# Kernel tuning notes

Measured on AMD Instinct MI355X. Metric: run time of the kernel, lower is better.

## Reference

```python
import jax, jax.numpy as jnp
import numpy as np

B, S, D_IN, D_H = 8, 2048, 512, 512

def setup_inputs() -> dict:
    key = jax.random.key(0)
    ks = jax.random.split(key, 7)
    s = 1.0 / np.sqrt(D_IN)
    return {
        "x": jax.random.normal(ks[0], (B, S, D_IN), dtype=jnp.float32),
        "Wq": jax.random.uniform(ks[1], (D_H, D_IN), jnp.float32, -s, s),
        "bq": jax.random.uniform(ks[2], (D_H,), jnp.float32, -s, s),
        "Wk": jax.random.uniform(ks[3], (D_H, D_IN), jnp.float32, -s, s),
        "bk": jax.random.uniform(ks[4], (D_H,), jnp.float32, -s, s),
        "Wv": jax.random.uniform(ks[5], (D_H, D_IN), jnp.float32, -s, s),
        "bv": jax.random.uniform(ks[6], (D_H,), jnp.float32, -s, s),
    }

def reference(x, Wq, bq, Wk, bk, Wv, bv):
    # torch Linear: y = x @ W.T + b
    Q = jnp.einsum('bsd,hd->bsh', x, Wq) + bq
    K = jnp.einsum('bsd,hd->bsh', x, Wk) + bk
    V = jnp.einsum('bsd,hd->bsh', x, Wv) + bv
    scale = jnp.sqrt(jnp.asarray(D_H, dtype=x.dtype))
    scores = jnp.einsum('bqh,bkh->bqk', Q, K) / scale  # [B,S,S]
    attn = jax.nn.softmax(scores, axis=-1)
    return jnp.einsum('bqk,bkh->bqh', attn, V)
```

## Files before the change

kernel.cpp:

```cpp
#include <hip/hip_runtime.h>
#include <hip/hip_bf16.h>
#include <cstdint>

#define B_   8
#define S_   2048
#define DIN  512
#define DH   512

typedef __attribute__((ext_vector_type(8))) short  short8;
typedef __attribute__((ext_vector_type(4))) short  short4_;
typedef __attribute__((ext_vector_type(4))) float  float4_;

__device__ inline unsigned short f2bf(float f) {
    union { float f; unsigned u; } v; v.f = f;
    unsigned u = v.u;
    u += 0x7fffu + ((u >> 16) & 1u);
    return (unsigned short)(u >> 16);
}

__device__ inline void gload_lds16(const void* g, void* l) {
    __builtin_amdgcn_global_load_lds(
        (const __attribute__((address_space(1))) void*)g,
        (__attribute__((address_space(3))) void*)l, 16, 0, 0);
}

template <int C>
__device__ inline float fdpp(float x) {
    return __int_as_float(__builtin_amdgcn_update_dpp(0, __float_as_int(x), C, 0xF, 0xF, true));
}
__device__ inline float rsum16(float v) {
    v += fdpp<0x140>(v);
    v += fdpp<0x141>(v);
    v += fdpp<27>(v);
    v += fdpp<177>(v);
    return v;
}

__global__ __launch_bounds__(256) void conv_bf16(
    const float* __restrict__ x,
    const float* __restrict__ Wq, const float* __restrict__ Wk, const float* __restrict__ Wv,
    unsigned short* __restrict__ xb, unsigned short* __restrict__ wb)
{
    const int NX4 = (B_ * S_ * DIN) / 4;
    const int NW4 = (DH * DIN) / 4;
    const int total = NX4 + 3 * NW4;
    for (int i = blockIdx.x * blockDim.x + threadIdx.x; i < total;
         i += gridDim.x * blockDim.x) {
        const float4_* src; unsigned short* dst; int j;
        if (i < NX4)             { src = (const float4_*)x;  dst = xb;            j = i; }
        else if (i < NX4 + NW4)  { src = (const float4_*)Wq; dst = wb;            j = i - NX4; }
        else if (i < NX4 + 2*NW4){ src = (const float4_*)Wk; dst = wb + DH*DIN;   j = i - NX4 - NW4; }
        else                     { src = (const float4_*)Wv; dst = wb + 2*DH*DIN; j = i - NX4 - 2*NW4; }
        float4_ v = src[j];
        short4_ o;
        o[0] = (short)f2bf(v[0]); o[1] = (short)f2bf(v[1]);
        o[2] = (short)f2bf(v[2]); o[3] = (short)f2bf(v[3]);
        ((short4_*)dst)[j] = o;
    }
}

__global__ __launch_bounds__(256) void qkv_gemm(
    const unsigned short* __restrict__ xb,
    const unsigned short* __restrict__ wb,
    const float* __restrict__ bq, const float* __restrict__ bk, const float* __restrict__ bv,
    unsigned short* __restrict__ qws, unsigned short* __restrict__ kws,
    unsigned short* __restrict__ vt2)
{
    __shared__ __align__(16) unsigned short smem[17408];

    const int flat = blockIdx.y * 128 + blockIdx.x;
    const int swz  = (flat & 7) * 192 + (flat >> 3);
    const int tm   = swz / 12;
    const int tc   = swz % 12;
    const int mat  = tc >> 2;
    const int nb   = (tc & 3) * 128;
    const int tid  = threadIdx.x;
    const int w    = tid >> 6;
    const int lane = tid & 63;
    const int l15  = lane & 15;
    const int quad = lane >> 4;
    const int wm   = (w & 1) * 64;
    const int wn   = (w >> 1) * 64;
    const int m0   = tm * 128;

    const unsigned short* wmat = wb + (size_t)mat * DH * DIN;

    float4_ zero = {0.f, 0.f, 0.f, 0.f};
    float4_ acc[4][4];
    #pragma unroll
    for (int i = 0; i < 4; i++)
        #pragma unroll
        for (int j = 0; j < 4; j++) acc[i][j] = zero;

    const int lr = lane >> 2;
    const int lb = (lane & 3) * 16;

    auto stage = [&](int kk, int bufi) {
        unsigned short* Ab = smem + bufi * 8192;
        unsigned short* Bb = smem + 4096 + bufi * 8192;
        #pragma unroll
        for (int c = 0; c < 2; c++) {
            int r = w * 32 + c * 16;
            const unsigned char* gA = (const unsigned char*)(xb + (size_t)(m0 + r) * DIN + kk);
            gload_lds16(gA + (size_t)lr * (DIN * 2) + lb, (void*)(Ab + r * 32));
            const unsigned char* gB = (const unsigned char*)(wmat + (size_t)(nb + r) * DIN + kk);
            gload_lds16(gB + (size_t)lr * (DIN * 2) + lb, (void*)(Bb + r * 32));
        }
    };

    stage(0, 0);
    for (int ki = 0; ki < 16; ki++) {
        __syncthreads();
        if (ki < 15) stage((ki + 1) * 32, (ki + 1) & 1);
        const unsigned short* Ab = smem + (ki & 1) * 8192;
        const unsigned short* Bb = smem + 4096 + (ki & 1) * 8192;
        short8 af[4], bf[4];
        #pragma unroll
        for (int mt = 0; mt < 4; mt++)
            af[mt] = *(const short8*)(Ab + (wm + mt * 16 + l15) * 32 + quad * 8);
        #pragma unroll
        for (int nt = 0; nt < 4; nt++)
            bf[nt] = *(const short8*)(Bb + (wn + nt * 16 + l15) * 32 + quad * 8);
        #pragma unroll
        for (int mt = 0; mt < 4; mt++)
            #pragma unroll
            for (int nt = 0; nt < 4; nt++)
                acc[mt][nt] = __builtin_amdgcn_mfma_f32_16x16x32_bf16(af[mt], bf[nt], acc[mt][nt], 0, 0, 0);
    }

    if (mat < 2) {
        const float* bias  = (mat == 0) ? bq : bk;
        const float  scale = (mat == 0) ? 0.06375870430742225f : 1.0f;
        unsigned short* dst = (mat == 0) ? qws : kws;
        #pragma unroll
        for (int nt = 0; nt < 4; nt++) {
            int n = nb + wn + nt * 16 + l15;
            float bv_ = bias[n];
            #pragma unroll
            for (int mt = 0; mt < 4; mt++) {
                #pragma unroll
                for (int r = 0; r < 4; r++) {
                    int m = m0 + wm + mt * 16 + quad * 4 + r;
                    dst[(size_t)m * DH + n] = f2bf((acc[mt][nt][r] + bv_) * scale);
                }
            }
        }
    } else {
        __syncthreads();
        unsigned short* trans = smem;
        #pragma unroll
        for (int nt = 0; nt < 4; nt++) {
            int dloc = wn + nt * 16 + l15;
            float bv_ = bv[nb + dloc];
            #pragma unroll
            for (int mt = 0; mt < 4; mt++) {
                short4_ pk;
                #pragma unroll
                for (int r = 0; r < 4; r++) pk[r] = (short)f2bf(acc[mt][nt][r] + bv_);
                *(short4_*)(trans + dloc * 136 + wm + mt * 16 + quad * 4) = pk;
            }
        }
        __syncthreads();
        int dl   = tid >> 1;
        int h    = tid & 1;
        int dh_g = nb + dl;
        int bi   = m0 >> 11;
        int tile0 = (m0 & 2047) >> 4;
        unsigned char* vt2b = (unsigned char*)vt2;
        #pragma unroll
        for (int t = 0; t < 4; t++) {
            int tl = h * 4 + t;
            const uint4* c = (const uint4*)(trans + dl * 136 + tl * 16);
            unsigned char* dst = vt2b + ((size_t)(bi * 128 + tile0 + tl) << 14) + dh_g * 32;
            ((uint4*)dst)[0] = c[0];
            ((uint4*)dst)[1] = c[1];
        }
    }
}

__global__ __launch_bounds__(512, 2) void attn(
    const unsigned short* __restrict__ qws,
    const unsigned short* __restrict__ kws,
    const unsigned short* __restrict__ vt2,
    float* __restrict__ out)
{
    __shared__ __align__(16) unsigned char smem[76288];

    const int bid  = blockIdx.x;
    const int b    = bid & 7;
    const int qt_b = bid >> 3;
    const int tid  = threadIdx.x;
    const int w    = tid >> 6;
    const int g    = w >> 2;
    const int wl   = w & 3;
    const int lane = tid & 63;
    const int l15  = lane & 15;
    const int quad = lane >> 4;

    const int qrow0  = b * S_ + qt_b * 64;
    const int myqrow = qrow0 + wl * 16;

    const unsigned short* kgrp = kws + (size_t)(b * S_ + g * 1024) * DH;
    const unsigned char*  vtb  = (const unsigned char*)vt2;

    unsigned char* kb    = smem + g * 32768;
    unsigned char* pbase = smem + 65536 + g * 5120;
    float*         lbuf  = (float*)(smem + 75776);

    short8 qf[16];
    {
        const short8* qp = (const short8*)(qws + (size_t)(myqrow + l15) * DH);
        #pragma unroll
        for (int ksi = 0; ksi < 16; ksi++) qf[ksi] = qp[ksi * 4 + quad];
    }

    float4_ zero = {0.f, 0.f, 0.f, 0.f};
    float4_ o[16];
    #pragma unroll
    for (int i = 0; i < 16; i++) o[i] = zero;
    float l_[4] = {0.f, 0.f, 0.f, 0.f};

    short8 vreg[4];

    auto stageK = [&](int n, int bufi) {
        #pragma unroll
        for (int i = 0; i < 4; i++) {
            int row = wl * 4 + i;
            const unsigned char* gp =
                (const unsigned char*)(kgrp + (size_t)(n * 16 + row) * DH);
            gload_lds16(gp + ((lane ^ (row & 7)) << 4),
                        kb + bufi * 16384 + row * 1024);
        }
    };

    auto loadV = [&](int n) {
        const unsigned char* base = vtb
            + ((size_t)(b * 128 + (quad >> 1) * 64 + n) << 14) + (quad & 1) * 16;
        #pragma unroll
        for (int dht = 0; dht < 4; dht++)
            vreg[dht] = *(const short8*)(base + (size_t)(w * 64 + dht * 16 + l15) * 32);
    };

    auto doPV = [&](int bufi) {
        const unsigned char* pq = smem + 65536 + (quad >> 1) * 5120
                                + bufi * 2560 + (quad & 1) * 16;
        short8 pa[4];
        #pragma unroll
        for (int qt = 0; qt < 4; qt++)
            pa[qt] = *(const short8*)(pq + (qt * 16 + l15) * 40);
        #pragma unroll
        for (int dht = 0; dht < 4; dht++) {
            #pragma unroll
            for (int qt = 0; qt < 4; qt++)
                o[qt * 4 + dht] = __builtin_amdgcn_mfma_f32_16x16x32_bf16(pa[qt], vreg[dht], o[qt * 4 + dht], 0, 0, 0);
        }
    };

    stageK(0, 0);

    for (int it = 0; it < 64; it++) {
        __syncthreads();

        if (it) loadV(it - 1);
        if (it < 63) stageK(it + 1, (it + 1) & 1);

        const unsigned char* kt_ = kb + (it & 1) * 16384;
        float4_ s0 = zero, s1 = zero;
        #pragma unroll
        for (int ksi = 0; ksi < 16; ksi += 2) {
            short8 k0 = *(const short8*)(kt_ + l15 * 1024 + ((( ksi      * 4 + quad) ^ (l15 & 7)) << 4));
            short8 k1 = *(const short8*)(kt_ + l15 * 1024 + ((((ksi + 1) * 4 + quad) ^ (l15 & 7)) << 4));
            s0 = __builtin_amdgcn_mfma_f32_16x16x32_bf16(qf[ksi],     k0, s0, 0, 0, 0);
            s1 = __builtin_amdgcn_mfma_f32_16x16x32_bf16(qf[ksi + 1], k1, s1, 0, 0, 0);
        }
        float4_ sc = s0 + s1;

        unsigned short* pp = (unsigned short*)(pbase + (it & 1) * 2560);
        #pragma unroll
        for (int r = 0; r < 4; r++) {
            float p = __builtin_exp2f(sc[r]);
            l_[r] += p;
            pp[(wl * 16 + quad * 4 + r) * 20 + l15] = f2bf(p);
        }

        if (it) doPV((it - 1) & 1);
    }

    __syncthreads();
    loadV(63);
    doPV(1);

    float lsum[4];
    #pragma unroll
    for (int r = 0; r < 4; r++) lsum[r] = rsum16(l_[r]);
    if (l15 == 0) {
        #pragma unroll
        for (int r = 0; r < 4; r++)
            lbuf[g * 64 + wl * 16 + quad * 4 + r] = lsum[r];
    }
    __syncthreads();

    #pragma unroll
    for (int qt = 0; qt < 4; qt++) {
        float rl[4];
        #pragma unroll
        for (int r = 0; r < 4; r++) {
            int row = qt * 16 + quad * 4 + r;
            rl[r] = 1.f / (lbuf[row] + lbuf[64 + row]);
        }
        #pragma unroll
        for (int dht = 0; dht < 4; dht++)
            #pragma unroll
            for (int r = 0; r < 4; r++) {
                int row = qt * 16 + quad * 4 + r;
                out[(size_t)(qrow0 + row) * DH + w * 64 + dht * 16 + l15] =
                    o[qt * 4 + dht][r] * rl[r];
            }
    }
}

extern "C" void kernel_launch(void* const* d_in, const int* in_sizes, int n_in,
                              void* d_out, int out_size, void* d_ws, size_t ws_size,
                              hipStream_t stream) {
    const float* x  = (const float*)d_in[0];
    const float* Wq = (const float*)d_in[1];
    const float* bq = (const float*)d_in[2];
    const float* Wk = (const float*)d_in[3];
    const float* bk = (const float*)d_in[4];
    const float* Wv = (const float*)d_in[5];
    const float* bv = (const float*)d_in[6];
    float* out = (float*)d_out;

    unsigned short* qws = (unsigned short*)d_ws;
    unsigned short* kws = qws + (size_t)B_ * S_ * DH;
    unsigned short* vt2 = kws + (size_t)B_ * S_ * DH;

    unsigned short* xb = (unsigned short*)d_out;
    unsigned short* wb = xb + (size_t)B_ * S_ * DIN;

    conv_bf16<<<dim3(2048), dim3(256), 0, stream>>>(x, Wq, Wk, Wv, xb, wb);
    qkv_gemm<<<dim3(128, 12), dim3(256), 0, stream>>>(xb, wb, bq, bk, bv, qws, kws, vt2);
    attn<<<dim3(256), dim3(512), 0, stream>>>(qws, kws, vt2, out);
}
```

Baseline: 247.9 us.

## Split attention keys across two blocks and merge partial sums with atomics

Splits the key dimension of each attention block in two, doubling the grid from 256 to 512 blocks, with each block handling half of the keys. Unnormalised partial outputs and row sums are accumulated into the output and a workspace via float atomicAdd, then a separate kernel divides by the row sums. This targets poor CU fill on the 256-block grid. It costs a zeroing kernel, a merge kernel, extra global traffic for the full-size fp32 output atomics, and nondeterministic summation order. The launch bound is raised to 4 blocks per CU, but about 76 KB of LDS per block likely still limits residency.

```diff
diff --git a/kernel.cpp b/kernel.cpp
--- a/kernel.cpp
+++ b/kernel.cpp
@@ -178,29 +178,43 @@
     }
 }
 
-__global__ __launch_bounds__(512, 2) void attn(
+__global__ __launch_bounds__(256) void zero_f32(float4_* __restrict__ out4,
+                                                float4_* __restrict__ lws4)
+{
+    const int N1 = (B_ * S_ * DH) / 4;
+    const int N2 = (B_ * S_) / 4;
+    float4_ z = {0.f, 0.f, 0.f, 0.f};
+    for (int i = blockIdx.x * blockDim.x + threadIdx.x; i < N1 + N2;
+         i += gridDim.x * blockDim.x) {
+        if (i < N1) out4[i] = z;
+        else        lws4[i - N1] = z;
+    }
+}
+
+__global__ __launch_bounds__(512, 4) void attn(
     const unsigned short* __restrict__ qws,
     const unsigned short* __restrict__ kws,
     const unsigned short* __restrict__ vt2,
-    float* __restrict__ out)
+    float* __restrict__ out, float* __restrict__ lws)
 {
     __shared__ __align__(16) unsigned char smem[76288];
 
-    const int bid  = blockIdx.x;
-    const int b    = bid & 7;
-    const int qt_b = bid >> 3;
-    const int tid  = threadIdx.x;
-    const int w    = tid >> 6;
-    const int g    = w >> 2;
-    const int wl   = w & 3;
-    const int lane = tid & 63;
-    const int l15  = lane & 15;
-    const int quad = lane >> 4;
+    const int bid   = blockIdx.x;
+    const int b     = bid & 7;
+    const int split = (bid >> 3) & 1;
+    const int qt_b  = bid >> 4;
+    const int tid   = threadIdx.x;
+    const int w     = tid >> 6;
+    const int g     = w >> 2;
+    const int wl    = w & 3;
+    const int lane  = tid & 63;
+    const int l15   = lane & 15;
+    const int quad  = lane >> 4;
 
     const int qrow0  = b * S_ + qt_b * 64;
     const int myqrow = qrow0 + wl * 16;
 
-    const unsigned short* kgrp = kws + (size_t)(b * S_ + g * 1024) * DH;
+    const unsigned short* kgrp = kws + (size_t)(b * S_ + split * 1024 + g * 512) * DH;
     const unsigned char*  vtb  = (const unsigned char*)vt2;
 
     unsigned char* kb    = smem + g * 32768;
@@ -235,7 +249,8 @@
 
     auto loadV = [&](int n) {
         const unsigned char* base = vtb
-            + ((size_t)(b * 128 + (quad >> 1) * 64 + n) << 14) + (quad & 1) * 16;
+            + ((size_t)(b * 128 + split * 64 + (quad >> 1) * 32 + n) << 14)
+            + (quad & 1) * 16;
         #pragma unroll
         for (int dht = 0; dht < 4; dht++)
             vreg[dht] = *(const short8*)(base + (size_t)(w * 64 + dht * 16 + l15) * 32);
@@ -258,11 +273,11 @@
 
     stageK(0, 0);
 
-    for (int it = 0; it < 64; it++) {
+    for (int it = 0; it < 32; it++) {
         __syncthreads();
 
         if (it) loadV(it - 1);
-        if (it < 63) stageK(it + 1, (it + 1) & 1);
+        if (it < 31) stageK(it + 1, (it + 1) & 1);
 
         const unsigned char* kt_ = kb + (it & 1) * 16384;
         float4_ s0 = zero, s1 = zero;
@@ -287,7 +302,7 @@
     }
 
     __syncthreads();
-    loadV(63);
+    loadV(31);
     doPV(1);
 
     float lsum[4];
@@ -300,22 +315,31 @@
     }
     __syncthreads();
 
+    if (tid < 64)
+        atomicAdd(&lws[qrow0 + tid], lbuf[tid] + lbuf[64 + tid]);
+
     #pragma unroll
-    for (int qt = 0; qt < 4; qt++) {
-        float rl[4];
-        #pragma unroll
-        for (int r = 0; r < 4; r++) {
-            int row = qt * 16 + quad * 4 + r;
-            rl[r] = 1.f / (lbuf[row] + lbuf[64 + row]);
-        }
+    for (int qt = 0; qt < 4; qt++)
         #pragma unroll
         for (int dht = 0; dht < 4; dht++)
             #pragma unroll
             for (int r = 0; r < 4; r++) {
                 int row = qt * 16 + quad * 4 + r;
-                out[(size_t)(qrow0 + row) * DH + w * 64 + dht * 16 + l15] =
-                    o[qt * 4 + dht][r] * rl[r];
+                atomicAdd(&out[(size_t)(qrow0 + row) * DH + w * 64 + dht * 16 + l15],
+                          o[qt * 4 + dht][r]);
             }
+}
+
+__global__ __launch_bounds__(256) void merge_div(float4_* __restrict__ out4,
+                                                 const float* __restrict__ lws)
+{
+    const int N1 = (B_ * S_ * DH) / 4;
+    for (int i = blockIdx.x * blockDim.x + threadIdx.x; i < N1;
+         i += gridDim.x * blockDim.x) {
+        float rl = 1.f / lws[i >> 7];
+        float4_ v = out4[i];
+        v[0] *= rl; v[1] *= rl; v[2] *= rl; v[3] *= rl;
+        out4[i] = v;
     }
 }
 
@@ -334,11 +358,14 @@
     unsigned short* qws = (unsigned short*)d_ws;
     unsigned short* kws = qws + (size_t)B_ * S_ * DH;
     unsigned short* vt2 = kws + (size_t)B_ * S_ * DH;
+    float*          lws = (float*)(vt2 + (size_t)8 * 128 * 8192);
 
     unsigned short* xb = (unsigned short*)d_out;
     unsigned short* wb = xb + (size_t)B_ * S_ * DIN;
 
     conv_bf16<<<dim3(2048), dim3(256), 0, stream>>>(x, Wq, Wk, Wv, xb, wb);
     qkv_gemm<<<dim3(128, 12), dim3(256), 0, stream>>>(xb, wb, bq, bk, bv, qws, kws, vt2);
-    attn<<<dim3(256), dim3(512), 0, stream>>>(qws, kws, vt2, out);
-}
+    zero_f32<<<dim3(1024), dim3(256), 0, stream>>>((float4_*)out, (float4_*)lws);
+    attn<<<dim3(512), dim3(512), 0, stream>>>(qws, kws, vt2, out, lws);
+    merge_div<<<dim3(1024), dim3(256), 0, stream>>>((float4_*)out, lws);
+}
```

New measurement: 555.6 us. 124% more time.

## Load QKV GEMM fragments directly from global memory instead of LDS staging

Applied to the files above, without the earlier changes.

The QKV projection GEMM no longer stages A and B tiles through double-buffered LDS with async global-to-LDS loads and barriers. Each lane now loads its MFMA fragments straight from global memory, relying on L2/L1 for reuse across waves, with the k-loop unrolled by 4 and launch bounds raised to request 3 blocks per CU. This removes barriers and LDS traffic but adds redundant global loads, since the same tile rows are fetched by multiple waves, and exposes load latency that the LDS pipeline used to hide.

```diff
diff --git a/kernel.cpp b/kernel.cpp
--- a/kernel.cpp
+++ b/kernel.cpp
@@ -59,7 +59,7 @@
     }
 }
 
-__global__ __launch_bounds__(256) void qkv_gemm(
+__global__ __launch_bounds__(256, 3) void qkv_gemm(
     const unsigned short* __restrict__ xb,
     const unsigned short* __restrict__ wb,
     const float* __restrict__ bq, const float* __restrict__ bk, const float* __restrict__ bv,
@@ -92,35 +92,23 @@
         #pragma unroll
         for (int j = 0; j < 4; j++) acc[i][j] = zero;
 
-    const int lr = lane >> 2;
-    const int lb = (lane & 3) * 16;
-
-    auto stage = [&](int kk, int bufi) {
-        unsigned short* Ab = smem + bufi * 8192;
-        unsigned short* Bb = smem + 4096 + bufi * 8192;
-        #pragma unroll
-        for (int c = 0; c < 2; c++) {
-            int r = w * 32 + c * 16;
-            const unsigned char* gA = (const unsigned char*)(xb + (size_t)(m0 + r) * DIN + kk);
-            gload_lds16(gA + (size_t)lr * (DIN * 2) + lb, (void*)(Ab + r * 32));
-            const unsigned char* gB = (const unsigned char*)(wmat + (size_t)(nb + r) * DIN + kk);
-            gload_lds16(gB + (size_t)lr * (DIN * 2) + lb, (void*)(Bb + r * 32));
-        }
-    };
-
-    stage(0, 0);
+    const unsigned short* Ar[4];
+    const unsigned short* Br[4];
+    #pragma unroll
+    for (int mt = 0; mt < 4; mt++)
+        Ar[mt] = xb + (size_t)(m0 + wm + mt * 16 + l15) * DIN + quad * 8;
+    #pragma unroll
+    for (int nt = 0; nt < 4; nt++)
+        Br[nt] = wmat + (size_t)(nb + wn + nt * 16 + l15) * DIN + quad * 8;
+
+    #pragma unroll 4
     for (int ki = 0; ki < 16; ki++) {
-        __syncthreads();
-        if (ki < 15) stage((ki + 1) * 32, (ki + 1) & 1);
-        const unsigned short* Ab = smem + (ki & 1) * 8192;
-        const unsigned short* Bb = smem + 4096 + (ki & 1) * 8192;
+        const int kk = ki * 32;
         short8 af[4], bf[4];
         #pragma unroll
-        for (int mt = 0; mt < 4; mt++)
-            af[mt] = *(const short8*)(Ab + (wm + mt * 16 + l15) * 32 + quad * 8);
-        #pragma unroll
-        for (int nt = 0; nt < 4; nt++)
-            bf[nt] = *(const short8*)(Bb + (wn + nt * 16 + l15) * 32 + quad * 8);
+        for (int mt = 0; mt < 4; mt++) af[mt] = *(const short8*)(Ar[mt] + kk);
+        #pragma unroll
+        for (int nt = 0; nt < 4; nt++) bf[nt] = *(const short8*)(Br[nt] + kk);
         #pragma unroll
         for (int mt = 0; mt < 4; mt++)
             #pragma unroll
```

After: 318.2 us. 28.4% more time.
